# Kernel tuning notes

Measured on AMD Instinct MI355X. Metric: run time of the kernel, lower is better.

The kernel has to match this reference:

```python
import jax, jax.numpy as jnp
import numpy as np

N_NODES = 50000
DIM = 128
N_EDGES = 800000
N_UID = 4096
ORDER = 3
LN_EPS = 1e-5


def setup_inputs() -> dict:
    key = jax.random.key(0)
    ks = jax.random.split(key, 6)
    scale = 1.0 / np.sqrt(DIM)
    embedding = jax.random.normal(ks[0], (N_NODES, DIM), jnp.float32) * np.sqrt(2.0 / DIM)  # kaiming-ish
    W = jax.random.normal(ks[1], (ORDER, DIM, DIM), jnp.float32) * scale
    b = jnp.zeros((ORDER, DIM), jnp.float32)
    gamma = jnp.ones((ORDER, DIM), jnp.float32)
    beta = jnp.zeros((ORDER, DIM), jnp.float32)
    src = jax.random.randint(ks[2], (N_EDGES,), 0, N_NODES, jnp.int32)
    dst = jax.random.randint(ks[3], (N_EDGES,), 0, N_NODES, jnp.int32)
    uid = jax.random.randint(ks[4], (N_UID,), 0, N_NODES, jnp.int32)
    return {"embedding": embedding, "W": W, "b": b, "gamma": gamma,
            "beta": beta, "src": src, "dst": dst, "uid": uid}


def _layer_norm(x, g, bta):
    mu = jnp.mean(x, axis=-1, keepdims=True)
    var = jnp.var(x, axis=-1, keepdims=True)
    return (x - mu) * jax.lax.rsqrt(var + LN_EPS) * g + bta


def reference(embedding, W, b, gamma, beta, src, dst, uid):
    # in-degree per destination node (DGL 'gcn' aggregator uses in_degrees)
    deg = jax.ops.segment_sum(jnp.ones((src.shape[0],), embedding.dtype), dst,
                              num_segments=N_NODES)  # [N]
    inv = (1.0 / (deg + 1.0))[:, None]  # [N,1]
    feats = embedding
    for i in range(ORDER):
        # gather source features, scatter-sum into destinations
        neigh = jax.ops.segment_sum(feats[src], dst, num_segments=N_NODES)  # [N,D]
        h = (neigh + feats) * inv                    # gcn-style mean incl. self
        h = jnp.einsum('nd,ed->ne', h, W[i]) + b[i]  # fc_neigh
        feats = jax.nn.elu(_layer_norm(h, gamma[i], beta[i]))
    return feats[uid]  # [N_UID, D]
```

## Files before the change

kernel.cpp:

```cpp
#include <hip/hip_runtime.h>
#include <math.h>

typedef unsigned int   uint;
typedef unsigned short ushort;

#define N_NODES 50000
#define DIM     128
#define N_EDGES 800000
#define N_UID   4096
#define LN_EPS  1e-5f
#define RST     132
#define XST     136
#define NBUCK   196
#define PCHUNK  4096

typedef __attribute__((ext_vector_type(8))) short bf16x8;
typedef __attribute__((ext_vector_type(4))) float f32x4;
typedef __attribute__((ext_vector_type(2))) float f32x2;
typedef __attribute__((ext_vector_type(4))) uint  u32x4;

__device__ __forceinline__ float bf_lo(uint u) { return __builtin_bit_cast(float, u << 16); }
__device__ __forceinline__ float bf_hi(uint u) { return __builtin_bit_cast(float, u & 0xffff0000u); }
__device__ __forceinline__ uint pack_bf16(float a, float b) {
    uint ua = __builtin_bit_cast(uint, a);
    uint ub = __builtin_bit_cast(uint, b);
    uint ra = (ua + 0x7fffu + ((ua >> 16) & 1u)) >> 16;
    uint rb = (ub + 0x7fffu + ((ub >> 16) & 1u)) >> 16;
    return ra | (rb << 16);
}

__global__ __launch_bounds__(256) void prep_kernel(const float* __restrict__ emb, ushort* __restrict__ E,
                                                   const float* __restrict__ W, ushort* __restrict__ WB,
                                                   int* __restrict__ bhist,
                                                   ushort* __restrict__ T1, ushort* __restrict__ T2,
                                                   int* __restrict__ mark, int* __restrict__ cnt) {
    int i = blockIdx.x * 256 + threadIdx.x;
    if (i < N_NODES * DIM / 4) {
        const float4 v = ((const float4*)emb)[i];
        uint2 p;
        p.x = pack_bf16(v.x, v.y);
        p.y = pack_bf16(v.z, v.w);
        ((uint2*)E)[i] = p;
    }
    if (i < 3 * DIM * DIM / 4) {
        const float4 v = ((const float4*)W)[i];
        uint2 p;
        p.x = pack_bf16(v.x, v.y);
        p.y = pack_bf16(v.z, v.w);
        ((uint2*)WB)[i] = p;
    }
    if (i < NBUCK) bhist[i] = 0;
    if (i < N_NODES) mark[i] = 0;
    if (i == 0) cnt[0] = 0;
    if (i < DIM / 4) {
        const uint2 z = make_uint2(0u, 0u);
        ((uint2*)(E  + (size_t)N_NODES * DIM))[i] = z;
        ((uint2*)(T1 + (size_t)N_NODES * DIM))[i] = z;
        ((uint2*)(T2 + (size_t)N_NODES * DIM))[i] = z;
    }
}

__global__ __launch_bounds__(256) void bhist_kernel(const int* __restrict__ dst, int* __restrict__ bhist) {
    __shared__ int h[256];
    const int t = threadIdx.x;
    h[t] = 0;
    __syncthreads();
    for (int e = blockIdx.x * 256 + t; e < N_EDGES; e += gridDim.x * 256)
        atomicAdd(&h[dst[e] >> 8], 1);
    __syncthreads();
    if (t < NBUCK && h[t]) atomicAdd(&bhist[t], h[t]);
}

__global__ __launch_bounds__(256) void bscan_kernel(const int* __restrict__ bhist, int* __restrict__ bbase,
                                                    int* __restrict__ bcur, int* __restrict__ off) {
    __shared__ int sh[256];
    const int t = threadIdx.x;
    const int v = (t < NBUCK) ? bhist[t] : 0;
    sh[t] = v;
    __syncthreads();
    for (int o = 1; o < 256; o <<= 1) {
        int x = (t >= o) ? sh[t - o] : 0;
        __syncthreads();
        sh[t] += x;
        __syncthreads();
    }
    const int excl = sh[t] - v;
    if (t < NBUCK) { bbase[t] = excl; bcur[t] = excl; }
    if (t == NBUCK - 1) bbase[NBUCK] = excl + v;
    if (t == 0) off[N_NODES] = N_EDGES;
}

__global__ __launch_bounds__(256) void part_kernel(const int* __restrict__ src, const int* __restrict__ dst,
                                                   int* __restrict__ bcur, int* __restrict__ pak) {
    __shared__ int h[256];
    __shared__ int base[256];
    __shared__ int cur[256];
    const int t  = threadIdx.x;
    const int e0 = blockIdx.x * PCHUNK;
    const int e1 = min(e0 + PCHUNK, N_EDGES);
    h[t] = 0;
    __syncthreads();
    for (int i = e0 + t; i < e1; i += 256)
        atomicAdd(&h[dst[i] >> 8], 1);
    __syncthreads();
    if (t < NBUCK && h[t]) base[t] = atomicAdd(&bcur[t], h[t]);
    cur[t] = 0;
    __syncthreads();
    for (int i = e0 + t; i < e1; i += 256) {
        const int s = src[i], d = dst[i];
        const int b = d >> 8;
        const int q = atomicAdd(&cur[b], 1);
        pak[base[b] + q] = (s << 8) | (d & 255);
    }
}

__global__ __launch_bounds__(256) void bucket_kernel(const int* __restrict__ pak, const int* __restrict__ bbase,
                                                     int* __restrict__ off, int* __restrict__ csr) {
    __shared__ int cnt[256];
    __shared__ int pos[256];
    const int b = blockIdx.x, t = threadIdx.x;
    const int e0 = bbase[b], e1 = bbase[b + 1], m = e1 - e0;
    cnt[t] = 0;
    __syncthreads();
    for (int i = t; i < m; i += 256) atomicAdd(&cnt[pak[e0 + i] & 255], 1);
    __syncthreads();
    const int v = cnt[t];
    pos[t] = v;
    __syncthreads();
    for (int o = 1; o < 256; o <<= 1) {
        int x = (t >= o) ? pos[t - o] : 0;
        __syncthreads();
        pos[t] += x;
        __syncthreads();
    }
    const int excl = pos[t] - v;
    const int node = b * 256 + t;
    if (node < N_NODES) off[node] = e0 + excl;
    __syncthreads();
    pos[t] = excl;
    __syncthreads();
    for (int i = t; i < m; i += 256) {
        const int p = pak[e0 + i];
        const int q = atomicAdd(&pos[p & 255], 1);
        csr[e0 + q] = p >> 8;
    }
}

__global__ __launch_bounds__(256) void mark_kernel(const int* __restrict__ uid, const int* __restrict__ off,
                                                   const int* __restrict__ csr, int* __restrict__ mark) {
    const int i = blockIdx.x * 256 + threadIdx.x;
    if (i >= N_UID) return;
    const int n = uid[i];
    mark[n] = 1;
    const int d0 = off[n], d1 = off[n + 1];
    for (int e = d0; e < d1; ++e) mark[csr[e]] = 1;
}

__global__ __launch_bounds__(256) void compact_kernel(const int* __restrict__ mark, int* __restrict__ wl,
                                                      int* __restrict__ cnt) {
    const int i = blockIdx.x * 256 + threadIdx.x;
    if (i < N_NODES && mark[i]) wl[atomicAdd(cnt, 1)] = i;
}

template <bool OUT_BF16, bool OUT_BY_NODE>
__global__ __launch_bounds__(512) void layer_kernel(
    const ushort* __restrict__ fin, void* __restrict__ fout,
    const int* __restrict__ off, const int* __restrict__ csr,
    const int* __restrict__ uidmap, const ushort* __restrict__ wb,
    const float* __restrict__ bias, const float* __restrict__ gamma,
    const float* __restrict__ beta, int nrows, const int* __restrict__ nrows_dyn)
{
    __shared__ ushort xs[32 * XST];
    __shared__ float  ys[32 * RST];
    const int t = threadIdx.x;
    const int nr = nrows_dyn ? *nrows_dyn : nrows;
    const int rows = blockIdx.x * 32;
    if (rows >= nr) return;

    {
        const int lx   = t & 15;
        const int st   = t >> 4;
        const int slot = rows + st;
        const bool valid = slot < nr;
        int n = 0;
        if (valid) n = uidmap ? uidmap[slot] : slot;
        const uint4 q0 = ((const uint4*)(fin + (size_t)n * DIM))[lx];
        const int d0 = off[n];
        int d1 = off[n + 1];
        if (!valid) d1 = d0;
        const int deg = d1 - d0;

        f32x2 a[4];
        a[0] = f32x2{bf_lo(q0.x), bf_hi(q0.x)};
        a[1] = f32x2{bf_lo(q0.y), bf_hi(q0.y)};
        a[2] = f32x2{bf_lo(q0.z), bf_hi(q0.z)};
        a[3] = f32x2{bf_lo(q0.w), bf_hi(q0.w)};

        const int rounds = (deg + 7) >> 3;
        int id[8];
        int e = d0;
        if (rounds > 0) {
            #pragma unroll
            for (int k = 0; k < 8; ++k) {
                const int ee = e + k;
                const int c = csr[ee];
                id[k] = (ee < d1) ? c : N_NODES;
            }
        }
        for (int r = 0; r < rounds; ++r) {
            uint4 v[8];
            #pragma unroll
            for (int k = 0; k < 8; ++k)
                v[k] = ((const uint4*)(fin + (size_t)id[k] * DIM))[lx];
            if (r + 1 < rounds) {
                #pragma unroll
                for (int k = 0; k < 8; ++k) {
                    const int ee = e + 8 + k;
                    const int c = csr[ee];
                    id[k] = (ee < d1) ? c : N_NODES;
                }
            }
            #pragma unroll
            for (int k = 0; k < 8; ++k) {
                a[0] += f32x2{bf_lo(v[k].x), bf_hi(v[k].x)};
                a[1] += f32x2{bf_lo(v[k].y), bf_hi(v[k].y)};
                a[2] += f32x2{bf_lo(v[k].z), bf_hi(v[k].z)};
                a[3] += f32x2{bf_lo(v[k].w), bf_hi(v[k].w)};
            }
            e += 8;
        }

        const float iv = 1.0f / (float)(deg + 1);
        uint4 p;
        p.x = pack_bf16(a[0].x * iv, a[0].y * iv);
        p.y = pack_bf16(a[1].x * iv, a[1].y * iv);
        p.z = pack_bf16(a[2].x * iv, a[2].y * iv);
        p.w = pack_bf16(a[3].x * iv, a[3].y * iv);
        *((uint4*)(xs + st * XST + lx * 8)) = p;
    }
    __syncthreads();

    {
        const int wave = t >> 6, lane = t & 63;
        const int row_off = (wave >> 2) * 16;
        const int col_off = (wave & 3) * 32;
        const int lm   = lane & 15;
        const int quad = lane >> 4;
        f32x4 acc[2] = {f32x4{0,0,0,0}, f32x4{0,0,0,0}};
        const ushort* xrow = xs + (row_off + lm) * XST + quad * 8;
        const ushort* __restrict__ wrow = wb + (size_t)(col_off + lm) * DIM + quad * 8;
        #pragma unroll
        for (int kk = 0; kk < 4; ++kk) {
            const bf16x8 af = __builtin_bit_cast(bf16x8, *(const u32x4*)(xrow + kk * 32));
            #pragma unroll
            for (int c = 0; c < 2; ++c) {
                const bf16x8 bfr = __builtin_bit_cast(bf16x8,
                    *(const u32x4*)(wrow + (size_t)c * 16 * DIM + kk * 32));
                acc[c] = __builtin_amdgcn_mfma_f32_16x16x32_bf16(af, bfr, acc[c], 0, 0, 0);
            }
        }
        #pragma unroll
        for (int c = 0; c < 2; ++c) {
            #pragma unroll
            for (int r = 0; r < 4; ++r)
                ys[(row_off + quad * 4 + r) * RST + col_off + c * 16 + lm] = acc[c][r];
        }
    }
    __syncthreads();

    {
        const int r   = t >> 4;
        const int seg = t & 15;
        const int db  = seg * 8;
        const float* yr = ys + r * RST + db;
        float vs[8];
        {
            const float4 y0 = ((const float4*)yr)[0];
            const float4 y1 = ((const float4*)yr)[1];
            const float4 b0 = ((const float4*)(bias + db))[0];
            const float4 b1 = ((const float4*)(bias + db))[1];
            vs[0] = y0.x + b0.x; vs[1] = y0.y + b0.y; vs[2] = y0.z + b0.z; vs[3] = y0.w + b0.w;
            vs[4] = y1.x + b1.x; vs[5] = y1.y + b1.y; vs[6] = y1.z + b1.z; vs[7] = y1.w + b1.w;
        }
        float s1 = 0.0f, s2 = 0.0f;
        #pragma unroll
        for (int i = 0; i < 8; ++i) { s1 += vs[i]; s2 += vs[i] * vs[i]; }
        #pragma unroll
        for (int m = 1; m < 16; m <<= 1) {
            s1 += __shfl_xor(s1, m);
            s2 += __shfl_xor(s2, m);
        }
        const float mu  = s1 * (1.0f / 128.0f);
        const float var = s2 * (1.0f / 128.0f) - mu * mu;
        const float rs  = rsqrtf(var + LN_EPS);
        float ov[8];
        {
            const float4 g0 = ((const float4*)(gamma + db))[0];
            const float4 g1 = ((const float4*)(gamma + db))[1];
            const float4 t0 = ((const float4*)(beta + db))[0];
            const float4 t1 = ((const float4*)(beta + db))[1];
            float z;
            z = (vs[0] - mu) * rs * g0.x + t0.x; ov[0] = (z > 0.0f) ? z : __expf(z) - 1.0f;
            z = (vs[1] - mu) * rs * g0.y + t0.y; ov[1] = (z > 0.0f) ? z : __expf(z) - 1.0f;
            z = (vs[2] - mu) * rs * g0.z + t0.z; ov[2] = (z > 0.0f) ? z : __expf(z) - 1.0f;
            z = (vs[3] - mu) * rs * g0.w + t0.w; ov[3] = (z > 0.0f) ? z : __expf(z) - 1.0f;
            z = (vs[4] - mu) * rs * g1.x + t1.x; ov[4] = (z > 0.0f) ? z : __expf(z) - 1.0f;
            z = (vs[5] - mu) * rs * g1.y + t1.y; ov[5] = (z > 0.0f) ? z : __expf(z) - 1.0f;
            z = (vs[6] - mu) * rs * g1.z + t1.z; ov[6] = (z > 0.0f) ? z : __expf(z) - 1.0f;
            z = (vs[7] - mu) * rs * g1.w + t1.w; ov[7] = (z > 0.0f) ? z : __expf(z) - 1.0f;
        }
        const int slot = rows + r;
        if (slot < nr) {
            const int orow = OUT_BY_NODE ? uidmap[slot] : slot;
            if (OUT_BF16) {
                uint4 p;
                p.x = pack_bf16(ov[0], ov[1]);
                p.y = pack_bf16(ov[2], ov[3]);
                p.z = pack_bf16(ov[4], ov[5]);
                p.w = pack_bf16(ov[6], ov[7]);
                *((uint4*)((ushort*)fout + (size_t)orow * DIM + db)) = p;
            } else {
                float* op = (float*)fout + (size_t)orow * DIM + db;
                ((float4*)op)[0] = make_float4(ov[0], ov[1], ov[2], ov[3]);
                ((float4*)op)[1] = make_float4(ov[4], ov[5], ov[6], ov[7]);
            }
        }
    }
}

extern "C" void kernel_launch(void* const* d_in, const int* in_sizes, int n_in,
                              void* d_out, int out_size, void* d_ws, size_t ws_size,
                              hipStream_t stream) {
    const float* emb   = (const float*)d_in[0];
    const float* W     = (const float*)d_in[1];
    const float* bias  = (const float*)d_in[2];
    const float* gamma = (const float*)d_in[3];
    const float* beta  = (const float*)d_in[4];
    const int*   src   = (const int*)d_in[5];
    const int*   dst   = (const int*)d_in[6];
    const int*   uid   = (const int*)d_in[7];

    const size_t FROW = (size_t)(N_NODES + 1) * DIM;
    ushort* E    = (ushort*)d_ws;
    ushort* T1   = E + FROW;
    ushort* T2   = T1 + FROW;
    ushort* WB   = T2 + FROW;
    int*    off  = (int*)(WB + 3 * DIM * DIM);
    int*    bhist = off + (N_NODES + 4);
    int*    bbase = bhist + 256;
    int*    bcur  = bbase + 260;
    int*    mark  = bcur + 256;
    int*    wl    = mark + N_NODES;
    int*    cnt   = wl + N_NODES;
    int*    pak   = cnt + 4;
    int*    csr   = pak + N_EDGES;

    prep_kernel<<<(N_NODES * DIM / 4 + 255) / 256, 256, 0, stream>>>(emb, E, W, WB, bhist, T1, T2, mark, cnt);
    bhist_kernel<<<512, 256, 0, stream>>>(dst, bhist);
    bscan_kernel<<<1, 256, 0, stream>>>(bhist, bbase, bcur, off);
    part_kernel<<<(N_EDGES + PCHUNK - 1) / PCHUNK, 256, 0, stream>>>(src, dst, bcur, pak);
    bucket_kernel<<<NBUCK, 256, 0, stream>>>(pak, bbase, off, csr);
    mark_kernel<<<(N_UID + 255) / 256, 256, 0, stream>>>(uid, off, csr, mark);
    compact_kernel<<<(N_NODES + 255) / 256, 256, 0, stream>>>(mark, wl, cnt);

    const int lblk = (N_NODES + 31) / 32;

    layer_kernel<true, false><<<lblk, 512, 0, stream>>>(E, T1, off, csr, nullptr, WB,
                                                        bias, gamma, beta, N_NODES, nullptr);
    layer_kernel<true, true><<<lblk, 512, 0, stream>>>(T1, T2, off, csr, wl, WB + DIM * DIM,
                                                       bias + DIM, gamma + DIM, beta + DIM,
                                                       0, cnt);
    layer_kernel<false, false><<<N_UID / 32, 512, 0, stream>>>(T2, (float*)d_out, off, csr, uid,
                                                               WB + 2 * DIM * DIM, bias + 2 * DIM,
                                                               gamma + 2 * DIM, beta + 2 * DIM,
                                                               N_UID, nullptr);
}
```

Baseline: 231.4 us.

## Fuse preprocessing into one cooperative kernel and double-buffer neighbor gathers

Seven preprocessing kernels (bf16 conversion, bucket histogram, scan, partition, bucket sort, marking, compaction) are merged into a single cooperative kernel that uses grid-wide syncs, removing per-launch gaps. Marking and worklist compaction are combined through atomicExch. The partition chunk size is halved to fit the 784-block grid. In the layer kernel the neighbor gather now keeps two 8-edge batches in flight, and launch bounds ask for four blocks per CU. The trade-offs are grid.sync overhead, a grid limited to what can be co-resident, higher register pressure from double buffering, and a worklist order that is no longer deterministic.

```diff
diff --git a/kernel.cpp b/kernel.cpp
--- a/kernel.cpp
+++ b/kernel.cpp
@@ -1,5 +1,8 @@
 #include <hip/hip_runtime.h>
+#include <hip/hip_cooperative_groups.h>
 #include <math.h>
+
+namespace cg = cooperative_groups;
 
 typedef unsigned int   uint;
 typedef unsigned short ushort;
@@ -12,7 +15,9 @@
 #define RST     132
 #define XST     136
 #define NBUCK   196
-#define PCHUNK  4096
+#define PCHUNK  2048
+#define NCHUNK  ((N_EDGES + PCHUNK - 1) / PCHUNK)
+#define PGRID   784
 
 typedef __attribute__((ext_vector_type(8))) short bf16x8;
 typedef __attribute__((ext_vector_type(4))) float f32x4;
@@ -29,141 +34,137 @@
     return ra | (rb << 16);
 }
 
-__global__ __launch_bounds__(256) void prep_kernel(const float* __restrict__ emb, ushort* __restrict__ E,
-                                                   const float* __restrict__ W, ushort* __restrict__ WB,
-                                                   int* __restrict__ bhist,
-                                                   ushort* __restrict__ T1, ushort* __restrict__ T2,
-                                                   int* __restrict__ mark, int* __restrict__ cnt) {
-    int i = blockIdx.x * 256 + threadIdx.x;
-    if (i < N_NODES * DIM / 4) {
-        const float4 v = ((const float4*)emb)[i];
+struct PArgs {
+    const float* emb; const float* W; const int* src; const int* dst; const int* uid;
+    ushort* E; ushort* WB; ushort* T1; ushort* T2;
+    int* off; int* bhist; int* bbase; int* bcur; int* mark; int* wl; int* cnt;
+    int* pak; int* csr;
+};
+
+__global__ __launch_bounds__(256) void preproc_kernel(PArgs A) {
+    cg::grid_group grid = cg::this_grid();
+    __shared__ int S[768];
+    const int t = threadIdx.x;
+    const int b = blockIdx.x;
+    const int gsz  = PGRID * 256;
+    const int gid0 = b * 256 + t;
+
+    for (int i = gid0; i < N_NODES * DIM / 4; i += gsz) {
+        const float4 v = ((const float4*)A.emb)[i];
         uint2 p;
         p.x = pack_bf16(v.x, v.y);
         p.y = pack_bf16(v.z, v.w);
-        ((uint2*)E)[i] = p;
-    }
-    if (i < 3 * DIM * DIM / 4) {
-        const float4 v = ((const float4*)W)[i];
+        ((uint2*)A.E)[i] = p;
+    }
+    if (gid0 < 3 * DIM * DIM / 4) {
+        const float4 v = ((const float4*)A.W)[gid0];
         uint2 p;
         p.x = pack_bf16(v.x, v.y);
         p.y = pack_bf16(v.z, v.w);
-        ((uint2*)WB)[i] = p;
-    }
-    if (i < NBUCK) bhist[i] = 0;
-    if (i < N_NODES) mark[i] = 0;
-    if (i == 0) cnt[0] = 0;
-    if (i < DIM / 4) {
+        ((uint2*)A.WB)[gid0] = p;
+    }
+    for (int i = gid0; i < N_NODES; i += gsz) A.mark[i] = 0;
+    if (gid0 < 256) A.bhist[gid0] = 0;
+    if (gid0 == 0) A.cnt[0] = 0;
+    if (gid0 < DIM / 4) {
         const uint2 z = make_uint2(0u, 0u);
-        ((uint2*)(E  + (size_t)N_NODES * DIM))[i] = z;
-        ((uint2*)(T1 + (size_t)N_NODES * DIM))[i] = z;
-        ((uint2*)(T2 + (size_t)N_NODES * DIM))[i] = z;
+        ((uint2*)(A.E  + (size_t)N_NODES * DIM))[gid0] = z;
+        ((uint2*)(A.T1 + (size_t)N_NODES * DIM))[gid0] = z;
+        ((uint2*)(A.T2 + (size_t)N_NODES * DIM))[gid0] = z;
+    }
+    grid.sync();
+
+    S[t] = 0;
+    __syncthreads();
+    for (int e = gid0; e < N_EDGES; e += gsz) atomicAdd(&S[A.dst[e] >> 8], 1);
+    __syncthreads();
+    if (t < NBUCK && S[t]) atomicAdd(&A.bhist[t], S[t]);
+    grid.sync();
+
+    if (b == 0) {
+        const int v = (t < NBUCK) ? A.bhist[t] : 0;
+        S[t] = v;
+        __syncthreads();
+        for (int o = 1; o < 256; o <<= 1) {
+            int x = (t >= o) ? S[t - o] : 0;
+            __syncthreads();
+            S[t] += x;
+            __syncthreads();
+        }
+        const int excl = S[t] - v;
+        if (t < NBUCK) { A.bbase[t] = excl; A.bcur[t] = excl; }
+        if (t == NBUCK - 1) A.bbase[NBUCK] = excl + v;
+        if (t == 0) A.off[N_NODES] = N_EDGES;
+    }
+    grid.sync();
+
+    if (b < NCHUNK) {
+        int* h    = S;
+        int* base = S + 256;
+        int* cur  = S + 512;
+        const int e0 = b * PCHUNK;
+        const int e1 = min(e0 + PCHUNK, N_EDGES);
+        h[t] = 0;
+        __syncthreads();
+        for (int i = e0 + t; i < e1; i += 256)
+            atomicAdd(&h[A.dst[i] >> 8], 1);
+        __syncthreads();
+        if (t < NBUCK && h[t]) base[t] = atomicAdd(&A.bcur[t], h[t]);
+        cur[t] = 0;
+        __syncthreads();
+        for (int i = e0 + t; i < e1; i += 256) {
+            const int s = A.src[i], d = A.dst[i];
+            const int bk = d >> 8;
+            const int q = atomicAdd(&cur[bk], 1);
+            A.pak[base[bk] + q] = (s << 8) | (d & 255);
+        }
+    }
+    grid.sync();
+
+    if (b < NBUCK) {
+        int* cnt_ = S;
+        int* pos  = S + 256;
+        const int e0 = A.bbase[b], e1 = A.bbase[b + 1], m = e1 - e0;
+        cnt_[t] = 0;
+        __syncthreads();
+        for (int i = t; i < m; i += 256) atomicAdd(&cnt_[A.pak[e0 + i] & 255], 1);
+        __syncthreads();
+        const int v = cnt_[t];
+        pos[t] = v;
+        __syncthreads();
+        for (int o = 1; o < 256; o <<= 1) {
+            int x = (t >= o) ? pos[t - o] : 0;
+            __syncthreads();
+            pos[t] += x;
+            __syncthreads();
+        }
+        const int excl = pos[t] - v;
+        const int node = b * 256 + t;
+        if (node < N_NODES) A.off[node] = e0 + excl;
+        __syncthreads();
+        pos[t] = excl;
+        __syncthreads();
+        for (int i = t; i < m; i += 256) {
+            const int p = A.pak[e0 + i];
+            const int q = atomicAdd(&pos[p & 255], 1);
+            A.csr[e0 + q] = p >> 8;
+        }
+    }
+    grid.sync();
+
+    for (int i = gid0; i < N_UID; i += gsz) {
+        const int n = A.uid[i];
+        if (atomicExch(&A.mark[n], 1) == 0) A.wl[atomicAdd(A.cnt, 1)] = n;
+        const int d0 = A.off[n], d1 = A.off[n + 1];
+        for (int e = d0; e < d1; ++e) {
+            const int vv = A.csr[e];
+            if (atomicExch(&A.mark[vv], 1) == 0) A.wl[atomicAdd(A.cnt, 1)] = vv;
+        }
     }
 }
 
-__global__ __launch_bounds__(256) void bhist_kernel(const int* __restrict__ dst, int* __restrict__ bhist) {
-    __shared__ int h[256];
-    const int t = threadIdx.x;
-    h[t] = 0;
-    __syncthreads();
-    for (int e = blockIdx.x * 256 + t; e < N_EDGES; e += gridDim.x * 256)
-        atomicAdd(&h[dst[e] >> 8], 1);
-    __syncthreads();
-    if (t < NBUCK && h[t]) atomicAdd(&bhist[t], h[t]);
-}
-
-__global__ __launch_bounds__(256) void bscan_kernel(const int* __restrict__ bhist, int* __restrict__ bbase,
-                                                    int* __restrict__ bcur, int* __restrict__ off) {
-    __shared__ int sh[256];
-    const int t = threadIdx.x;
-    const int v = (t < NBUCK) ? bhist[t] : 0;
-    sh[t] = v;
-    __syncthreads();
-    for (int o = 1; o < 256; o <<= 1) {
-        int x = (t >= o) ? sh[t - o] : 0;
-        __syncthreads();
-        sh[t] += x;
-        __syncthreads();
-    }
-    const int excl = sh[t] - v;
-    if (t < NBUCK) { bbase[t] = excl; bcur[t] = excl; }
-    if (t == NBUCK - 1) bbase[NBUCK] = excl + v;
-    if (t == 0) off[N_NODES] = N_EDGES;
-}
-
-__global__ __launch_bounds__(256) void part_kernel(const int* __restrict__ src, const int* __restrict__ dst,
-                                                   int* __restrict__ bcur, int* __restrict__ pak) {
-    __shared__ int h[256];
-    __shared__ int base[256];
-    __shared__ int cur[256];
-    const int t  = threadIdx.x;
-    const int e0 = blockIdx.x * PCHUNK;
-    const int e1 = min(e0 + PCHUNK, N_EDGES);
-    h[t] = 0;
-    __syncthreads();
-    for (int i = e0 + t; i < e1; i += 256)
-        atomicAdd(&h[dst[i] >> 8], 1);
-    __syncthreads();
-    if (t < NBUCK && h[t]) base[t] = atomicAdd(&bcur[t], h[t]);
-    cur[t] = 0;
-    __syncthreads();
-    for (int i = e0 + t; i < e1; i += 256) {
-        const int s = src[i], d = dst[i];
-        const int b = d >> 8;
-        const int q = atomicAdd(&cur[b], 1);
-        pak[base[b] + q] = (s << 8) | (d & 255);
-    }
-}
-
-__global__ __launch_bounds__(256) void bucket_kernel(const int* __restrict__ pak, const int* __restrict__ bbase,
-                                                     int* __restrict__ off, int* __restrict__ csr) {
-    __shared__ int cnt[256];
-    __shared__ int pos[256];
-    const int b = blockIdx.x, t = threadIdx.x;
-    const int e0 = bbase[b], e1 = bbase[b + 1], m = e1 - e0;
-    cnt[t] = 0;
-    __syncthreads();
-    for (int i = t; i < m; i += 256) atomicAdd(&cnt[pak[e0 + i] & 255], 1);
-    __syncthreads();
-    const int v = cnt[t];
-    pos[t] = v;
-    __syncthreads();
-    for (int o = 1; o < 256; o <<= 1) {
-        int x = (t >= o) ? pos[t - o] : 0;
-        __syncthreads();
-        pos[t] += x;
-        __syncthreads();
-    }
-    const int excl = pos[t] - v;
-    const int node = b * 256 + t;
-    if (node < N_NODES) off[node] = e0 + excl;
-    __syncthreads();
-    pos[t] = excl;
-    __syncthreads();
-    for (int i = t; i < m; i += 256) {
-        const int p = pak[e0 + i];
-        const int q = atomicAdd(&pos[p & 255], 1);
-        csr[e0 + q] = p >> 8;
-    }
-}
-
-__global__ __launch_bounds__(256) void mark_kernel(const int* __restrict__ uid, const int* __restrict__ off,
-                                                   const int* __restrict__ csr, int* __restrict__ mark) {
-    const int i = blockIdx.x * 256 + threadIdx.x;
-    if (i >= N_UID) return;
-    const int n = uid[i];
-    mark[n] = 1;
-    const int d0 = off[n], d1 = off[n + 1];
-    for (int e = d0; e < d1; ++e) mark[csr[e]] = 1;
-}
-
-__global__ __launch_bounds__(256) void compact_kernel(const int* __restrict__ mark, int* __restrict__ wl,
-                                                      int* __restrict__ cnt) {
-    const int i = blockIdx.x * 256 + threadIdx.x;
-    if (i < N_NODES && mark[i]) wl[atomicAdd(cnt, 1)] = i;
-}
-
 template <bool OUT_BF16, bool OUT_BY_NODE>
-__global__ __launch_bounds__(512) void layer_kernel(
+__global__ __launch_bounds__(512, 4) void layer_kernel(
     const ushort* __restrict__ fin, void* __restrict__ fout,
     const int* __restrict__ off, const int* __restrict__ csr,
     const int* __restrict__ uidmap, const ushort* __restrict__ wb,
@@ -190,52 +191,48 @@
         if (!valid) d1 = d0;
         const int deg = d1 - d0;
 
-        f32x2 a[4];
-        a[0] = f32x2{bf_lo(q0.x), bf_hi(q0.x)};
-        a[1] = f32x2{bf_lo(q0.y), bf_hi(q0.y)};
-        a[2] = f32x2{bf_lo(q0.z), bf_hi(q0.z)};
-        a[3] = f32x2{bf_lo(q0.w), bf_hi(q0.w)};
+        f32x2 a0 = f32x2{bf_lo(q0.x), bf_hi(q0.x)};
+        f32x2 a1 = f32x2{bf_lo(q0.y), bf_hi(q0.y)};
+        f32x2 a2 = f32x2{bf_lo(q0.z), bf_hi(q0.z)};
+        f32x2 a3 = f32x2{bf_lo(q0.w), bf_hi(q0.w)};
 
         const int rounds = (deg + 7) >> 3;
-        int id[8];
         int e = d0;
-        if (rounds > 0) {
-            #pragma unroll
-            for (int k = 0; k < 8; ++k) {
-                const int ee = e + k;
-                const int c = csr[ee];
-                id[k] = (ee < d1) ? c : N_NODES;
+        int ida[8], idb[8];
+        uint4 va[8], vb[8];
+
+#define LIDS(ID, BASE) { _Pragma("unroll") for (int k = 0; k < 8; ++k) {        \
+            const int ee = (BASE) + k; const int c = csr[ee];                   \
+            ID[k] = (ee < d1) ? c : N_NODES; } }
+#define LVEC(VV, ID) { _Pragma("unroll") for (int k = 0; k < 8; ++k)            \
+            VV[k] = ((const uint4*)(fin + (size_t)ID[k] * DIM))[lx]; }
+#define ACC(VV) { _Pragma("unroll") for (int k = 0; k < 8; ++k) {               \
+            a0 += f32x2{bf_lo(VV[k].x), bf_hi(VV[k].x)};                        \
+            a1 += f32x2{bf_lo(VV[k].y), bf_hi(VV[k].y)};                        \
+            a2 += f32x2{bf_lo(VV[k].z), bf_hi(VV[k].z)};                        \
+            a3 += f32x2{bf_lo(VV[k].w), bf_hi(VV[k].w)}; } }
+
+        if (rounds > 0) { LIDS(ida, e);     LVEC(va, ida); }
+        if (rounds > 1) { LIDS(idb, e + 8); LVEC(vb, idb); }
+        for (int r = 0; r < rounds; r += 2) {
+            ACC(va);
+            if (r + 2 < rounds) { LIDS(ida, e + 16); LVEC(va, ida); }
+            if (r + 1 < rounds) {
+                ACC(vb);
+                if (r + 3 < rounds) { LIDS(idb, e + 24); LVEC(vb, idb); }
             }
-        }
-        for (int r = 0; r < rounds; ++r) {
-            uint4 v[8];
-            #pragma unroll
-            for (int k = 0; k < 8; ++k)
-                v[k] = ((const uint4*)(fin + (size_t)id[k] * DIM))[lx];
-            if (r + 1 < rounds) {
-                #pragma unroll
-                for (int k = 0; k < 8; ++k) {
-                    const int ee = e + 8 + k;
-                    const int c = csr[ee];
-                    id[k] = (ee < d1) ? c : N_NODES;
-                }
-            }
-            #pragma unroll
-            for (int k = 0; k < 8; ++k) {
-                a[0] += f32x2{bf_lo(v[k].x), bf_hi(v[k].x)};
-                a[1] += f32x2{bf_lo(v[k].y), bf_hi(v[k].y)};
-                a[2] += f32x2{bf_lo(v[k].z), bf_hi(v[k].z)};
-                a[3] += f32x2{bf_lo(v[k].w), bf_hi(v[k].w)};
-            }
-            e += 8;
-        }
+            e += 16;
+        }
+#undef LIDS
+#undef LVEC
+#undef ACC
 
         const float iv = 1.0f / (float)(deg + 1);
         uint4 p;
-        p.x = pack_bf16(a[0].x * iv, a[0].y * iv);
-        p.y = pack_bf16(a[1].x * iv, a[1].y * iv);
-        p.z = pack_bf16(a[2].x * iv, a[2].y * iv);
-        p.w = pack_bf16(a[3].x * iv, a[3].y * iv);
+        p.x = pack_bf16(a0.x * iv, a0.y * iv);
+        p.y = pack_bf16(a1.x * iv, a1.y * iv);
+        p.z = pack_bf16(a2.x * iv, a2.y * iv);
+        p.w = pack_bf16(a3.x * iv, a3.y * iv);
         *((uint4*)(xs + st * XST + lx * 8)) = p;
     }
     __syncthreads();
@@ -355,13 +352,14 @@
     int*    pak   = cnt + 4;
     int*    csr   = pak + N_EDGES;
 
-    prep_kernel<<<(N_NODES * DIM / 4 + 255) / 256, 256, 0, stream>>>(emb, E, W, WB, bhist, T1, T2, mark, cnt);
-    bhist_kernel<<<512, 256, 0, stream>>>(dst, bhist);
-    bscan_kernel<<<1, 256, 0, stream>>>(bhist, bbase, bcur, off);
-    part_kernel<<<(N_EDGES + PCHUNK - 1) / PCHUNK, 256, 0, stream>>>(src, dst, bcur, pak);
-    bucket_kernel<<<NBUCK, 256, 0, stream>>>(pak, bbase, off, csr);
-    mark_kernel<<<(N_UID + 255) / 256, 256, 0, stream>>>(uid, off, csr, mark);
-    compact_kernel<<<(N_NODES + 255) / 256, 256, 0, stream>>>(mark, wl, cnt);
+    PArgs pa;
+    pa.emb = emb; pa.W = W; pa.src = src; pa.dst = dst; pa.uid = uid;
+    pa.E = E; pa.WB = WB; pa.T1 = T1; pa.T2 = T2;
+    pa.off = off; pa.bhist = bhist; pa.bbase = bbase; pa.bcur = bcur;
+    pa.mark = mark; pa.wl = wl; pa.cnt = cnt; pa.pak = pak; pa.csr = csr;
+    void* params[1] = { (void*)&pa };
+    hipLaunchCooperativeKernel((const void*)preproc_kernel, dim3(PGRID), dim3(256),
+                               params, 0, stream);
 
     const int lblk = (N_NODES + 31) / 32;
 
```

Measured after the change: 709.2 us. +206.5%, slower.
